# Performance work log

Hardware: AMD Instinct MI355X
Metric: run time of the kernel (lower is better)

## Reference

```python
import jax, jax.numpy as jnp
import numpy as np

N_NODES = 50000
N_EDGES = 800000
IN_DIM = 256
NHID = 64
OUT_DIM = 64
DEPTH = 4
P = 2.0


def _gcn_conv(x, W, b, src, dst, n):
    # PyG GCNConv: xW, add self-loops, sym-normalize, aggregate src->dst, + bias
    xw = x @ W
    loop = jnp.arange(n)
    s = jnp.concatenate([src, loop])
    d = jnp.concatenate([dst, loop])
    deg = jax.ops.segment_sum(jnp.ones_like(d, dtype=xw.dtype), d, num_segments=n)
    dis = jnp.where(deg > 0, jax.lax.rsqrt(jnp.maximum(deg, 1.0)), 0.0)
    w = dis[s] * dis[d]  # [E+n]
    out = jax.ops.segment_sum(w[:, None] * xw[s], d, num_segments=n)
    return out + b


def _g2_gate(x, W, b, src, dst, n):
    xg = jax.nn.relu(_gcn_conv(x, W, b, src, dst, n))
    diff = jnp.abs(xg[src] - xg[dst]) ** P  # [E, nhid]
    sums = jax.ops.segment_sum(diff, src, num_segments=n)
    cnt = jax.ops.segment_sum(jnp.ones((src.shape[0],), dtype=x.dtype), src, num_segments=n)
    return jnp.tanh(sums / jnp.maximum(cnt, 1.0)[:, None])


def setup_inputs() -> dict:
    key = jax.random.key(0)
    ks = jax.random.split(key, 10)
    x = jax.random.normal(ks[0], (N_NODES, IN_DIM), dtype=jnp.float32)
    edge_index = jax.random.randint(ks[1], (2, N_EDGES), 0, N_NODES, dtype=jnp.int64 if jax.config.jax_enable_x64 else jnp.int32)
    s = 0.05
    return {
        "x": x,
        "edge_index": edge_index,
        "enc_w": jax.random.normal(ks[2], (IN_DIM, NHID), dtype=jnp.float32) * s,
        "enc_b": jnp.zeros((NHID,), dtype=jnp.float32),
        "conv_w": jax.random.normal(ks[3], (NHID, NHID), dtype=jnp.float32) * s,
        "conv_b": jnp.zeros((NHID,), dtype=jnp.float32),
        "gg_w": jax.random.normal(ks[4], (NHID, NHID), dtype=jnp.float32) * s,
        "gg_b": jnp.zeros((NHID,), dtype=jnp.float32),
        "dec_w": jax.random.normal(ks[5], (NHID, OUT_DIM), dtype=jnp.float32) * s,
        "dec_b": jnp.zeros((OUT_DIM,), dtype=jnp.float32),
    }


def reference(x, edge_index, enc_w, enc_b, conv_w, conv_b, gg_w, gg_b, dec_w, dec_b):
    n = x.shape[0]
    src, dst = edge_index[0], edge_index[1]
    # eval mode: dropouts are identity
    X = jax.nn.relu(x @ enc_w + enc_b)
    for _ in range(DEPTH):
        X_ = jax.nn.relu(_gcn_conv(X, conv_w, conv_b, src, dst, n))
        tau = _g2_gate(X, gg_w, gg_b, src, dst, n)
        X = (1.0 - tau) * X + tau * X_
    X = jax.nn.relu(X @ dec_w + dec_b)
    return X
```

## Files before the change

### kernel.cpp

```cpp
#include <hip/hip_runtime.h>
#include <math.h>

#define NN 50000
#define NE 800000
#define IND 256
#define NH 64
#define DEPTH 4
#define PART_DIV 6250
#define SB 49
#define EPP 100000


__device__ __forceinline__ unsigned short f2bf(float f) {
    unsigned int x = __float_as_uint(f);
    unsigned int r = (x + 0x7fffu + ((x >> 16) & 1u)) >> 16;
    return (unsigned short)r;
}
__device__ __forceinline__ unsigned int pack2bf(float lo, float hi) {
    return (unsigned int)f2bf(lo) | ((unsigned int)f2bf(hi) << 16);
}
__device__ __forceinline__ ushort4 f4_to_us4(float4 f) {
    ushort4 u;
    u.x = f2bf(f.x); u.y = f2bf(f.y); u.z = f2bf(f.z); u.w = f2bf(f.w);
    return u;
}
__device__ __forceinline__ void acc8(float* a, uint4 r) {
    a[0] += __uint_as_float(r.x << 16); a[1] += __uint_as_float(r.x & 0xffff0000u);
    a[2] += __uint_as_float(r.y << 16); a[3] += __uint_as_float(r.y & 0xffff0000u);
    a[4] += __uint_as_float(r.z << 16); a[5] += __uint_as_float(r.z & 0xffff0000u);
    a[6] += __uint_as_float(r.w << 16); a[7] += __uint_as_float(r.w & 0xffff0000u);
}
__device__ __forceinline__ void unpack8(float* a, uint4 r) {
    a[0] = __uint_as_float(r.x << 16); a[1] = __uint_as_float(r.x & 0xffff0000u);
    a[2] = __uint_as_float(r.y << 16); a[3] = __uint_as_float(r.y & 0xffff0000u);
    a[4] = __uint_as_float(r.z << 16); a[5] = __uint_as_float(r.z & 0xffff0000u);
    a[6] = __uint_as_float(r.w << 16); a[7] = __uint_as_float(r.w & 0xffff0000u);
}
__device__ __forceinline__ void accd8(float* a, const float* xg, uint4 r) {
    float e;
    e = xg[0] - __uint_as_float(r.x << 16);         a[0] += e * e;
    e = xg[1] - __uint_as_float(r.x & 0xffff0000u); a[1] += e * e;
    e = xg[2] - __uint_as_float(r.y << 16);         a[2] += e * e;
    e = xg[3] - __uint_as_float(r.y & 0xffff0000u); a[3] += e * e;
    e = xg[4] - __uint_as_float(r.z << 16);         a[4] += e * e;
    e = xg[5] - __uint_as_float(r.z & 0xffff0000u); a[5] += e * e;
    e = xg[6] - __uint_as_float(r.w << 16);         a[6] += e * e;
    e = xg[7] - __uint_as_float(r.w & 0xffff0000u); a[7] += e * e;
}
__device__ __forceinline__ float tanh_pos(float x) {
    float t = __expf(-2.f * x);
    return (1.f - t) / (1.f + t);
}


__global__ void count8(const int* __restrict__ src, const int* __restrict__ dst,
                       int* __restrict__ hin, int* __restrict__ hout,
                       int* __restrict__ lrin, int* __restrict__ lrout,
                       int nGroups) {
    int p = blockIdx.x & 7;
    int g = blockIdx.x >> 3;
    int* hi = hin + p * NN;
    int* ho = hout + p * NN;
    for (int i = g * 256 + threadIdx.x; i < EPP; i += nGroups * 256) {
        int e = p * EPP + i;
        int s = src[e], d = dst[e];
        lrin[e]  = atomicAdd(&hi[d], 1);
        lrout[e] = atomicAdd(&ho[s], 1);
    }
}

__global__ void reduce8(int* __restrict__ hin, int* __restrict__ hout,
                        int* __restrict__ degin, int* __restrict__ degout) {
    int i = blockIdx.x * blockDim.x + threadIdx.x;
    if (i >= NN) return;
    int run = 0;
#pragma unroll
    for (int p = 0; p < 8; ++p) {
        int t = hin[p * NN + i]; hin[p * NN + i] = run; run += t;
    }
    degin[i] = run;
    run = 0;
#pragma unroll
    for (int p = 0; p < 8; ++p) {
        int t = hout[p * NN + i]; hout[p * NN + i] = run; run += t;
    }
    degout[i] = run;
}

__global__ __launch_bounds__(512) void scan_p1(const int* __restrict__ in0,
                                               const int* __restrict__ in1,
                                               int* __restrict__ tmp,
                                               int* __restrict__ bsum) {
    int a = blockIdx.x / SB;
    int b = blockIdx.x % SB;
    const int* in = a ? in1 : in0;
    int t = threadIdx.x;
    int base = b * 1024 + t * 2;
    int v0 = (base < NN) ? in[base] : 0;
    int v1 = (base + 1 < NN) ? in[base + 1] : 0;
    int v = v0 + v1;
    int x = v;
#pragma unroll
    for (int off = 1; off < 64; off <<= 1) {
        int u = __shfl_up(x, off);
        if ((t & 63) >= off) x += u;
    }
    __shared__ int ws[8];
    int wid = t >> 6, lane = t & 63;
    if (lane == 63) ws[wid] = x;
    __syncthreads();
    if (t == 0) {
        int run = 0;
#pragma unroll
        for (int w = 0; w < 8; ++w) { int s = ws[w]; ws[w] = run; run += s; }
    }
    __syncthreads();
    x += ws[wid];
    int excl = x - v;
    if (base < NN) tmp[a * NN + base] = excl;
    if (base + 1 < NN) tmp[a * NN + base + 1] = excl + v0;
    if (t == 511) bsum[a * SB + b] = x;
}

__global__ __launch_bounds__(128) void scan_p2(int* __restrict__ bsum,
                                               int* __restrict__ out0,
                                               int* __restrict__ out1) {
    int t = threadIdx.x;
    int a = t >> 6, lane = t & 63;
    int v = (lane < SB) ? bsum[a * SB + lane] : 0;
    int x = v;
#pragma unroll
    for (int off = 1; off < 64; off <<= 1) {
        int u = __shfl_up(x, off);
        if (lane >= off) x += u;
    }
    if (lane < SB) bsum[a * SB + lane] = x - v;
    if (lane == SB - 1) {
        if (a == 0) out0[NN] = x; else out1[NN] = x;
    }
}

__global__ __launch_bounds__(512) void scan_p3(const int* __restrict__ tmp,
                                               const int* __restrict__ bsum,
                                               int* __restrict__ out0,
                                               int* __restrict__ out1) {
    int a = blockIdx.x / SB;
    int b = blockIdx.x % SB;
    int* out = a ? out1 : out0;
    int add = bsum[a * SB + b];
    int t = threadIdx.x;
    int base = b * 1024 + t * 2;
    if (base < NN) out[base] = tmp[a * NN + base] + add;
    if (base + 1 < NN) out[base + 1] = tmp[a * NN + base + 1] + add;
}

__global__ void init_node(const int* __restrict__ degin, const int* __restrict__ degout,
                          float* __restrict__ dis, float* __restrict__ cntf) {
    int i = blockIdx.x * blockDim.x + threadIdx.x;
    if (i < NN) {
        dis[i] = rsqrtf((float)(degin[i] + 1));
        int od = degout[i];
        cntf[i] = (float)(od > 0 ? od : 1);
    }
}

__global__ void fill_csr_part(const int* __restrict__ src, const int* __restrict__ dst,
                              const int* __restrict__ off_dst, const int* __restrict__ off_src,
                              const int* __restrict__ hin, const int* __restrict__ hout,
                              const int* __restrict__ lrin, const int* __restrict__ lrout,
                              int* __restrict__ srcs_by_dst, int* __restrict__ dsts_by_src,
                              int nGroups) {
    int q = blockIdx.x & 7;
    int g = blockIdx.x >> 3;
    for (int pe = 0; pe < 8; ++pe) {
        const int* bin = hin + pe * NN;
        const int* bout = hout + pe * NN;
        for (int i = g * 256 + threadIdx.x; i < EPP; i += nGroups * 256) {
            int e = pe * EPP + i;
            int s = src[e], d = dst[e];
            if (d / PART_DIV == q) srcs_by_dst[off_dst[d] + bin[d] + lrin[e]] = s;
            if (s / PART_DIV == q) dsts_by_src[off_src[s] + bout[s] + lrout[e]] = d;
        }
    }
}

template<int K, bool RELU, bool WSC>
__global__ __launch_bounds__(256) void gemm64b(const float* __restrict__ X,
                                               const float* __restrict__ W,
                                               const float* __restrict__ bias,
                                               const float* __restrict__ rowscale,
                                               float* __restrict__ out,
                                               unsigned short* __restrict__ xsc, int n) {
    __shared__ float Ws[64 * 64];
    __shared__ float Xs[64][68];
    int tid = threadIdx.x;
    int row0 = blockIdx.x * 64;
    int r16 = tid >> 4;
    int cg = tid & 15;
    float4 acc[4];
#pragma unroll
    for (int t = 0; t < 4; ++t) acc[t] = make_float4(0.f, 0.f, 0.f, 0.f);

    for (int kc = 0; kc < K; kc += 64) {
        const float4* W4 = (const float4*)(W + (size_t)kc * 64);
        float4* Ws4 = (float4*)Ws;
#pragma unroll
        for (int t = 0; t < 4; ++t) Ws4[tid + t * 256] = W4[tid + t * 256];
#pragma unroll
        for (int t = 0; t < 4; ++t) {
            int r = r16 + t * 16;
            int grow = row0 + r;
            float4 xv = make_float4(0.f, 0.f, 0.f, 0.f);
            if (grow < n) xv = *(const float4*)(X + (size_t)grow * K + kc + cg * 4);
            Xs[r][cg * 4 + 0] = xv.x; Xs[r][cg * 4 + 1] = xv.y;
            Xs[r][cg * 4 + 2] = xv.z; Xs[r][cg * 4 + 3] = xv.w;
        }
        __syncthreads();
#pragma unroll
        for (int k = 0; k < 64; ++k) {
            float4 w4 = ((const float4*)Ws)[k * 16 + cg];
#pragma unroll
            for (int t = 0; t < 4; ++t) {
                float xv = Xs[r16 + t * 16][k];
                acc[t].x += xv * w4.x; acc[t].y += xv * w4.y;
                acc[t].z += xv * w4.z; acc[t].w += xv * w4.w;
            }
        }
        __syncthreads();
    }

    float4 b4 = ((const float4*)bias)[cg];
#pragma unroll
    for (int t = 0; t < 4; ++t) {
        int row = row0 + r16 + t * 16;
        if (row < n) {
            float4 o;
            o.x = acc[t].x + b4.x; o.y = acc[t].y + b4.y;
            o.z = acc[t].z + b4.z; o.w = acc[t].w + b4.w;
            if (RELU) {
                o.x = fmaxf(o.x, 0.f); o.y = fmaxf(o.y, 0.f);
                o.z = fmaxf(o.z, 0.f); o.w = fmaxf(o.w, 0.f);
            }
            ((float4*)(out + (size_t)row * 64))[cg] = o;
            if (WSC) {
                float s = rowscale[row];
                float4 o2 = make_float4(o.x * s, o.y * s, o.z * s, o.w * s);
                ((ushort4*)(xsc + (size_t)row * 64))[cg] = f4_to_us4(o2);
            }
        }
    }
}

template<bool OUTBF>
__global__ __launch_bounds__(256) void gemm64z(const float* __restrict__ Z,
                                               const float* __restrict__ W,
                                               const float* __restrict__ bias,
                                               float* __restrict__ outf,
                                               unsigned short* __restrict__ outb, int n) {
    __shared__ float Ws[64 * 64];
    __shared__ float Xs[64][68];
    int tid = threadIdx.x;
    int row0 = blockIdx.x * 64;
    int r16 = tid >> 4;
    int cg = tid & 15;
    float4 acc[4];
#pragma unroll
    for (int t = 0; t < 4; ++t) acc[t] = make_float4(0.f, 0.f, 0.f, 0.f);

    {
        const float4* W4 = (const float4*)W;
        float4* Ws4 = (float4*)Ws;
#pragma unroll
        for (int t = 0; t < 4; ++t) Ws4[tid + t * 256] = W4[tid + t * 256];
#pragma unroll
        for (int t = 0; t < 4; ++t) {
            int r = r16 + t * 16;
            int gr = row0 + r;
            float4 xv = make_float4(0.f, 0.f, 0.f, 0.f);
            if (gr < n) xv = *(const float4*)(Z + (size_t)gr * 64 + cg * 4);
            Xs[r][cg * 4 + 0] = xv.x; Xs[r][cg * 4 + 1] = xv.y;
            Xs[r][cg * 4 + 2] = xv.z; Xs[r][cg * 4 + 3] = xv.w;
        }
        __syncthreads();
#pragma unroll
        for (int k = 0; k < 64; ++k) {
            float4 w4 = ((const float4*)Ws)[k * 16 + cg];
#pragma unroll
            for (int t = 0; t < 4; ++t) {
                float xv = Xs[r16 + t * 16][k];
                acc[t].x += xv * w4.x; acc[t].y += xv * w4.y;
                acc[t].z += xv * w4.z; acc[t].w += xv * w4.w;
            }
        }
    }

    float4 b4 = ((const float4*)bias)[cg];
#pragma unroll
    for (int t = 0; t < 4; ++t) {
        int row = row0 + r16 + t * 16;
        if (row < n) {
            float4 o;
            o.x = fmaxf(acc[t].x + b4.x, 0.f); o.y = fmaxf(acc[t].y + b4.y, 0.f);
            o.z = fmaxf(acc[t].z + b4.z, 0.f); o.w = fmaxf(acc[t].w + b4.w, 0.f);
            if (OUTBF) {
                ((ushort4*)(outb + (size_t)row * 64))[cg] = f4_to_us4(o);
            } else {
                ((float4*)(outf + (size_t)row * 64))[cg] = o;
            }
        }
    }
}

__global__ __launch_bounds__(256) void zgather(
    const unsigned short* __restrict__ Xbf,
    const int* __restrict__ off, const int* __restrict__ nbr,
    const float* __restrict__ dis, float* __restrict__ Z)
{
    int t = blockIdx.x * 256 + threadIdx.x;
    int node = t >> 3, l8 = t & 7;
    if (node >= NN) return;
    int lane = threadIdx.x & 63;
    int octbase = lane & ~7;
    const uint4* Xb = (const uint4*)Xbf;
    float a[8];
    unpack8(a, Xb[(size_t)node * 8 + l8]);
    int lo = off[node], hi = off[node + 1];
    int j = lo;
    for (; j + 7 < hi; j += 8) {
        int nv = nbr[j + l8];
        int s0 = __shfl(nv, octbase + 0), s1 = __shfl(nv, octbase + 1);
        int s2 = __shfl(nv, octbase + 2), s3 = __shfl(nv, octbase + 3);
        int s4 = __shfl(nv, octbase + 4), s5 = __shfl(nv, octbase + 5);
        int s6 = __shfl(nv, octbase + 6), s7 = __shfl(nv, octbase + 7);
        uint4 r0 = Xb[(size_t)s0 * 8 + l8];
        uint4 r1 = Xb[(size_t)s1 * 8 + l8];
        uint4 r2 = Xb[(size_t)s2 * 8 + l8];
        uint4 r3 = Xb[(size_t)s3 * 8 + l8];
        uint4 r4 = Xb[(size_t)s4 * 8 + l8];
        uint4 r5 = Xb[(size_t)s5 * 8 + l8];
        uint4 r6 = Xb[(size_t)s6 * 8 + l8];
        uint4 r7 = Xb[(size_t)s7 * 8 + l8];
        acc8(a, r0); acc8(a, r1); acc8(a, r2); acc8(a, r3);
        acc8(a, r4); acc8(a, r5); acc8(a, r6); acc8(a, r7);
    }
    for (; j + 3 < hi; j += 4) {
        int s0 = nbr[j], s1 = nbr[j + 1], s2 = nbr[j + 2], s3 = nbr[j + 3];
        uint4 r0 = Xb[(size_t)s0 * 8 + l8];
        uint4 r1 = Xb[(size_t)s1 * 8 + l8];
        uint4 r2 = Xb[(size_t)s2 * 8 + l8];
        uint4 r3 = Xb[(size_t)s3 * 8 + l8];
        acc8(a, r0); acc8(a, r1); acc8(a, r2); acc8(a, r3);
    }
    for (; j < hi; ++j) {
        acc8(a, Xb[(size_t)nbr[j] * 8 + l8]);
    }
    float di = dis[node];
    float* zp = Z + (size_t)node * 64 + l8 * 8;
    *(float4*)(zp)     = make_float4(di * a[0], di * a[1], di * a[2], di * a[3]);
    *(float4*)(zp + 4) = make_float4(di * a[4], di * a[5], di * a[6], di * a[7]);
}

__global__ __launch_bounds__(256) void gate_update8(
    const unsigned short* __restrict__ Cbf, const float* __restrict__ Xn,
    float* __restrict__ X, unsigned short* __restrict__ Xbf,
    const int* __restrict__ off, const int* __restrict__ nbr,
    const float* __restrict__ cntf, const float* __restrict__ dis)
{
    int t = blockIdx.x * 256 + threadIdx.x;
    int node = t >> 3, l8 = t & 7;
    if (node >= NN) return;
    int lane = threadIdx.x & 63;
    int octbase = lane & ~7;
    const uint4* Cb = (const uint4*)Cbf;
    float xg[8];
    unpack8(xg, Cb[(size_t)node * 8 + l8]);
    float a[8] = {0.f, 0.f, 0.f, 0.f, 0.f, 0.f, 0.f, 0.f};
    int lo = off[node], hi = off[node + 1];
    int j = lo;
    for (; j + 7 < hi; j += 8) {
        int nv = nbr[j + l8];
        int d0 = __shfl(nv, octbase + 0), d1 = __shfl(nv, octbase + 1);
        int d2 = __shfl(nv, octbase + 2), d3 = __shfl(nv, octbase + 3);
        int d4 = __shfl(nv, octbase + 4), d5 = __shfl(nv, octbase + 5);
        int d6 = __shfl(nv, octbase + 6), d7 = __shfl(nv, octbase + 7);
        uint4 r0 = Cb[(size_t)d0 * 8 + l8];
        uint4 r1 = Cb[(size_t)d1 * 8 + l8];
        uint4 r2 = Cb[(size_t)d2 * 8 + l8];
        uint4 r3 = Cb[(size_t)d3 * 8 + l8];
        uint4 r4 = Cb[(size_t)d4 * 8 + l8];
        uint4 r5 = Cb[(size_t)d5 * 8 + l8];
        uint4 r6 = Cb[(size_t)d6 * 8 + l8];
        uint4 r7 = Cb[(size_t)d7 * 8 + l8];
        accd8(a, xg, r0); accd8(a, xg, r1); accd8(a, xg, r2); accd8(a, xg, r3);
        accd8(a, xg, r4); accd8(a, xg, r5); accd8(a, xg, r6); accd8(a, xg, r7);
    }
    for (; j + 3 < hi; j += 4) {
        int d0 = nbr[j], d1 = nbr[j + 1], d2 = nbr[j + 2], d3 = nbr[j + 3];
        uint4 r0 = Cb[(size_t)d0 * 8 + l8];
        uint4 r1 = Cb[(size_t)d1 * 8 + l8];
        uint4 r2 = Cb[(size_t)d2 * 8 + l8];
        uint4 r3 = Cb[(size_t)d3 * 8 + l8];
        accd8(a, xg, r0); accd8(a, xg, r1); accd8(a, xg, r2); accd8(a, xg, r3);
    }
    for (; j < hi; ++j) {
        accd8(a, xg, Cb[(size_t)nbr[j] * 8 + l8]);
    }
    float inv = 1.f / cntf[node];
    float di = dis[node];
    const float* xop = X + (size_t)node * 64 + l8 * 8;
    const float* xnp = Xn + (size_t)node * 64 + l8 * 8;
    float o[8];
#pragma unroll
    for (int k = 0; k < 8; ++k) {
        float tau = tanh_pos(a[k] * inv);
        float xo = xop[k], xn = xnp[k];
        o[k] = xo + tau * (xn - xo);
    }
    float* xp = X + (size_t)node * 64 + l8 * 8;
    *(float4*)(xp)     = make_float4(o[0], o[1], o[2], o[3]);
    *(float4*)(xp + 4) = make_float4(o[4], o[5], o[6], o[7]);
    uint4 pk;
    pk.x = pack2bf(o[0] * di, o[1] * di);
    pk.y = pack2bf(o[2] * di, o[3] * di);
    pk.z = pack2bf(o[4] * di, o[5] * di);
    pk.w = pack2bf(o[6] * di, o[7] * di);
    ((uint4*)Xbf)[(size_t)node * 8 + l8] = pk;
}


extern "C" void kernel_launch(void* const* d_in, const int* in_sizes, int n_in,
                              void* d_out, int out_size, void* d_ws, size_t ws_size,
                              hipStream_t stream) {
    const float* x      = (const float*)d_in[0];
    const int*   ei     = (const int*)d_in[1];
    const float* enc_w  = (const float*)d_in[2];
    const float* enc_b  = (const float*)d_in[3];
    const float* conv_w = (const float*)d_in[4];
    const float* conv_b = (const float*)d_in[5];
    const float* gg_w   = (const float*)d_in[6];
    const float* gg_b   = (const float*)d_in[7];
    const float* dec_w  = (const float*)d_in[8];
    const float* dec_b  = (const float*)d_in[9];
    float* out = (float*)d_out;

    const int* src = ei;
    const int* dst = ei + NE;

    char* p = (char*)d_ws;
    auto alloc = [&](size_t bytes) -> void* {
        void* r = (void*)p;
        p += (bytes + 255) & ~(size_t)255;
        return r;
    };
    float* X   = (float*)alloc((size_t)NN * 64 * 4);
    float* Zb  = (float*)alloc((size_t)NN * 64 * 4);
    float* B   = (float*)alloc((size_t)NN * 64 * 4);
    unsigned short* Xbf = (unsigned short*)alloc((size_t)NN * 64 * 2);
    unsigned short* Cbf = (unsigned short*)alloc((size_t)NN * 64 * 2);
    float* dis  = (float*)alloc((size_t)NN * 4);
    float* cntf = (float*)alloc((size_t)NN * 4);
    int* degin   = (int*)alloc((size_t)NN * 4);
    int* degout  = (int*)alloc((size_t)NN * 4);
    int* off_dst = (int*)alloc((size_t)(NN + 1) * 4);
    int* off_src = (int*)alloc((size_t)(NN + 1) * 4);
    int* hin     = (int*)alloc((size_t)8 * NN * 4);
    int* hout    = (int*)alloc((size_t)8 * NN * 4);
    int* lrin    = (int*)alloc((size_t)NE * 4);
    int* lrout   = (int*)alloc((size_t)NE * 4);
    int* sbd     = (int*)alloc((size_t)NE * 4);
    int* dbs     = (int*)alloc((size_t)NE * 4);
    int* stmp    = (int*)alloc((size_t)2 * NN * 4);
    int* bsum    = (int*)alloc((size_t)2 * SB * 4);

    hipMemsetAsync(hin, 0, (size_t)8 * NN * 4, stream);
    hipMemsetAsync(hout, 0, (size_t)8 * NN * 4, stream);

    const int NB = (NN + 255) / 256;
    const int NGROUPS = 104;
    count8<<<8 * NGROUPS, 256, 0, stream>>>(src, dst, hin, hout, lrin, lrout, NGROUPS);
    reduce8<<<NB, 256, 0, stream>>>(hin, hout, degin, degout);
    scan_p1<<<2 * SB, 512, 0, stream>>>(degin, degout, stmp, bsum);
    scan_p2<<<1, 128, 0, stream>>>(bsum, off_dst, off_src);
    scan_p3<<<2 * SB, 512, 0, stream>>>(stmp, bsum, off_dst, off_src);
    init_node<<<NB, 256, 0, stream>>>(degin, degout, dis, cntf);
    fill_csr_part<<<8 * NGROUPS, 256, 0, stream>>>(src, dst, off_dst, off_src,
                                                   hin, hout, lrin, lrout,
                                                   sbd, dbs, NGROUPS);

    const int GB = (NN + 63) / 64;
    const int OB = ((NN * 8) + 255) / 256;

    gemm64b<IND, true, true><<<GB, 256, 0, stream>>>(x, enc_w, enc_b, dis, X, Xbf, NN);

    for (int l = 0; l < DEPTH; ++l) {
        zgather<<<OB, 256, 0, stream>>>(Xbf, off_dst, sbd, dis, Zb);
        gemm64z<false><<<GB, 256, 0, stream>>>(Zb, conv_w, conv_b, B, nullptr, NN);
        gemm64z<true><<<GB, 256, 0, stream>>>(Zb, gg_w, gg_b, nullptr, Cbf, NN);
        gate_update8<<<OB, 256, 0, stream>>>(Cbf, B, X, Xbf, off_src, dbs, cntf, dis);
    }

    gemm64b<NH, true, false><<<GB, 256, 0, stream>>>(X, dec_w, dec_b, nullptr, out, nullptr, NN);
}
```

Before: 685.2 us.

## Degree-sort node order for gathers, fuse dual GEMM, store B in bf16

Measured after the change: 651.8 us. 1.05x faster.

```diff
diff --git a/kernel.cpp b/kernel.cpp
--- a/kernel.cpp
+++ b/kernel.cpp
@@ -184,6 +184,61 @@
     }
 }
 
+__global__ void bucket_hist(const int* __restrict__ degin, const int* __restrict__ degout,
+                            int* __restrict__ ghin, int* __restrict__ ghout) {
+    __shared__ int lin[128], lout[128];
+    int t = threadIdx.x;
+    if (t < 128) { lin[t] = 0; lout[t] = 0; }
+    __syncthreads();
+    int i = blockIdx.x * 256 + t;
+    if (i < NN) {
+        atomicAdd(&lin[min(degin[i], 127)], 1);
+        atomicAdd(&lout[min(degout[i], 127)], 1);
+    }
+    __syncthreads();
+    if (t < 128) {
+        if (lin[t])  atomicAdd(&ghin[t],  lin[t]);
+        if (lout[t]) atomicAdd(&ghout[t], lout[t]);
+    }
+}
+
+__global__ void bucket_scan(const int* __restrict__ ghin, const int* __restrict__ ghout,
+                            int* __restrict__ curin, int* __restrict__ curout) {
+    __shared__ int a[128], b[128];
+    int t = threadIdx.x;
+    if (t < 128) a[t] = ghin[t]; else b[t - 128] = ghout[t - 128];
+    __syncthreads();
+    if (t == 0) { int run = 0; for (int k = 0; k < 128; ++k) { int v = a[k]; a[k] = run; run += v; } }
+    if (t == 1) { int run = 0; for (int k = 0; k < 128; ++k) { int v = b[k]; b[k] = run; run += v; } }
+    __syncthreads();
+    if (t < 128) curin[t] = a[t]; else curout[t - 128] = b[t - 128];
+}
+
+__global__ void bucket_scatter(const int* __restrict__ degin, const int* __restrict__ degout,
+                               int* __restrict__ curin, int* __restrict__ curout,
+                               int* __restrict__ order_in, int* __restrict__ order_out) {
+    __shared__ int lin[128], lout[128], basein[128], baseout[128];
+    int t = threadIdx.x;
+    if (t < 128) { lin[t] = 0; lout[t] = 0; }
+    __syncthreads();
+    int i = blockIdx.x * 256 + t;
+    int bi = 0, bo = 0, ri = 0, ro = 0;
+    if (i < NN) {
+        bi = min(degin[i], 127);  ri = atomicAdd(&lin[bi], 1);
+        bo = min(degout[i], 127); ro = atomicAdd(&lout[bo], 1);
+    }
+    __syncthreads();
+    if (t < 128) {
+        basein[t]  = lin[t]  ? atomicAdd(&curin[t],  lin[t])  : 0;
+        baseout[t] = lout[t] ? atomicAdd(&curout[t], lout[t]) : 0;
+    }
+    __syncthreads();
+    if (i < NN) {
+        order_in[basein[bi] + ri] = i;
+        order_out[baseout[bo] + ro] = i;
+    }
+}
+
 template<int K, bool RELU, bool WSC>
 __global__ __launch_bounds__(256) void gemm64b(const float* __restrict__ X,
                                                const float* __restrict__ W,
@@ -251,62 +306,65 @@
     }
 }
 
-template<bool OUTBF>
-__global__ __launch_bounds__(256) void gemm64z(const float* __restrict__ Z,
-                                               const float* __restrict__ W,
-                                               const float* __restrict__ bias,
-                                               float* __restrict__ outf,
-                                               unsigned short* __restrict__ outb, int n) {
-    __shared__ float Ws[64 * 64];
-    __shared__ float Xs[64][68];
+__global__ __launch_bounds__(256) void dualgemm32(
+    const float* __restrict__ Z,
+    const float* __restrict__ Wb, const float* __restrict__ bb,
+    const float* __restrict__ Wc, const float* __restrict__ bc,
+    unsigned short* __restrict__ Bbf, unsigned short* __restrict__ Cbf, int n)
+{
+    __shared__ float W2[64 * 128];
+    __shared__ float Xs[32][68];
     int tid = threadIdx.x;
-    int row0 = blockIdx.x * 64;
-    int r16 = tid >> 4;
-    int cg = tid & 15;
-    float4 acc[4];
-#pragma unroll
-    for (int t = 0; t < 4; ++t) acc[t] = make_float4(0.f, 0.f, 0.f, 0.f);
-
+    int row0 = blockIdx.x * 32;
     {
-        const float4* W4 = (const float4*)W;
-        float4* Ws4 = (float4*)Ws;
-#pragma unroll
-        for (int t = 0; t < 4; ++t) Ws4[tid + t * 256] = W4[tid + t * 256];
+        const float4* wb4 = (const float4*)Wb;
+        const float4* wc4 = (const float4*)Wc;
 #pragma unroll
         for (int t = 0; t < 4; ++t) {
-            int r = r16 + t * 16;
+            int idx = tid + t * 256;
+            int k = idx >> 4, c = (idx & 15) * 4;
+            *(float4*)&W2[k * 128 + c]      = wb4[idx];
+            *(float4*)&W2[k * 128 + 64 + c] = wc4[idx];
+        }
+#pragma unroll
+        for (int t = 0; t < 2; ++t) {
+            int idx = tid + t * 256;
+            int r = idx >> 4, c4 = idx & 15;
             int gr = row0 + r;
             float4 xv = make_float4(0.f, 0.f, 0.f, 0.f);
-            if (gr < n) xv = *(const float4*)(Z + (size_t)gr * 64 + cg * 4);
-            Xs[r][cg * 4 + 0] = xv.x; Xs[r][cg * 4 + 1] = xv.y;
-            Xs[r][cg * 4 + 2] = xv.z; Xs[r][cg * 4 + 3] = xv.w;
-        }
-        __syncthreads();
-#pragma unroll
-        for (int k = 0; k < 64; ++k) {
-            float4 w4 = ((const float4*)Ws)[k * 16 + cg];
-#pragma unroll
-            for (int t = 0; t < 4; ++t) {
-                float xv = Xs[r16 + t * 16][k];
-                acc[t].x += xv * w4.x; acc[t].y += xv * w4.y;
-                acc[t].z += xv * w4.z; acc[t].w += xv * w4.w;
-            }
-        }
-    }
-
-    float4 b4 = ((const float4*)bias)[cg];
+            if (gr < n) xv = *(const float4*)(Z + (size_t)gr * 64 + c4 * 4);
+            Xs[r][c4 * 4 + 0] = xv.x; Xs[r][c4 * 4 + 1] = xv.y;
+            Xs[r][c4 * 4 + 2] = xv.z; Xs[r][c4 * 4 + 3] = xv.w;
+        }
+    }
+    __syncthreads();
+
+    int r8 = tid >> 5;
+    int cg = tid & 31;
+    float4 acc[4];
+#pragma unroll
+    for (int t = 0; t < 4; ++t) acc[t] = make_float4(0.f, 0.f, 0.f, 0.f);
+#pragma unroll
+    for (int k = 0; k < 64; ++k) {
+        float4 w4 = *(const float4*)&W2[k * 128 + cg * 4];
+#pragma unroll
+        for (int t = 0; t < 4; ++t) {
+            float xv = Xs[r8 + t * 8][k];
+            acc[t].x += xv * w4.x; acc[t].y += xv * w4.y;
+            acc[t].z += xv * w4.z; acc[t].w += xv * w4.w;
+        }
+    }
+
+    float4 bv = (cg < 16) ? ((const float4*)bb)[cg] : ((const float4*)bc)[cg - 16];
 #pragma unroll
     for (int t = 0; t < 4; ++t) {
-        int row = row0 + r16 + t * 16;
+        int row = row0 + r8 + t * 8;
         if (row < n) {
             float4 o;
-            o.x = fmaxf(acc[t].x + b4.x, 0.f); o.y = fmaxf(acc[t].y + b4.y, 0.f);
-            o.z = fmaxf(acc[t].z + b4.z, 0.f); o.w = fmaxf(acc[t].w + b4.w, 0.f);
-            if (OUTBF) {
-                ((ushort4*)(outb + (size_t)row * 64))[cg] = f4_to_us4(o);
-            } else {
-                ((float4*)(outf + (size_t)row * 64))[cg] = o;
-            }
+            o.x = fmaxf(acc[t].x + bv.x, 0.f); o.y = fmaxf(acc[t].y + bv.y, 0.f);
+            o.z = fmaxf(acc[t].z + bv.z, 0.f); o.w = fmaxf(acc[t].w + bv.w, 0.f);
+            if (cg < 16) ((ushort4*)(Bbf + (size_t)row * 64))[cg]      = f4_to_us4(o);
+            else         ((ushort4*)(Cbf + (size_t)row * 64))[cg - 16] = f4_to_us4(o);
         }
     }
 }
@@ -314,24 +372,21 @@
 __global__ __launch_bounds__(256) void zgather(
     const unsigned short* __restrict__ Xbf,
     const int* __restrict__ off, const int* __restrict__ nbr,
-    const float* __restrict__ dis, float* __restrict__ Z)
+    const float* __restrict__ dis, const int* __restrict__ order,
+    float* __restrict__ Z)
 {
     int t = blockIdx.x * 256 + threadIdx.x;
-    int node = t >> 3, l8 = t & 7;
-    if (node >= NN) return;
-    int lane = threadIdx.x & 63;
-    int octbase = lane & ~7;
+    int idx = t >> 3, l8 = t & 7;
+    if (idx >= NN) return;
+    int node = order[idx];
     const uint4* Xb = (const uint4*)Xbf;
     float a[8];
     unpack8(a, Xb[(size_t)node * 8 + l8]);
     int lo = off[node], hi = off[node + 1];
     int j = lo;
     for (; j + 7 < hi; j += 8) {
-        int nv = nbr[j + l8];
-        int s0 = __shfl(nv, octbase + 0), s1 = __shfl(nv, octbase + 1);
-        int s2 = __shfl(nv, octbase + 2), s3 = __shfl(nv, octbase + 3);
-        int s4 = __shfl(nv, octbase + 4), s5 = __shfl(nv, octbase + 5);
-        int s6 = __shfl(nv, octbase + 6), s7 = __shfl(nv, octbase + 7);
+        int s0 = nbr[j],     s1 = nbr[j + 1], s2 = nbr[j + 2], s3 = nbr[j + 3];
+        int s4 = nbr[j + 4], s5 = nbr[j + 5], s6 = nbr[j + 6], s7 = nbr[j + 7];
         uint4 r0 = Xb[(size_t)s0 * 8 + l8];
         uint4 r1 = Xb[(size_t)s1 * 8 + l8];
         uint4 r2 = Xb[(size_t)s2 * 8 + l8];
@@ -361,16 +416,16 @@
 }
 
 __global__ __launch_bounds__(256) void gate_update8(
-    const unsigned short* __restrict__ Cbf, const float* __restrict__ Xn,
+    const unsigned short* __restrict__ Cbf, const unsigned short* __restrict__ Xnbf,
     float* __restrict__ X, unsigned short* __restrict__ Xbf,
     const int* __restrict__ off, const int* __restrict__ nbr,
-    const float* __restrict__ cntf, const float* __restrict__ dis)
+    const float* __restrict__ cntf, const float* __restrict__ dis,
+    const int* __restrict__ order)
 {
     int t = blockIdx.x * 256 + threadIdx.x;
-    int node = t >> 3, l8 = t & 7;
-    if (node >= NN) return;
-    int lane = threadIdx.x & 63;
-    int octbase = lane & ~7;
+    int idx = t >> 3, l8 = t & 7;
+    if (idx >= NN) return;
+    int node = order[idx];
     const uint4* Cb = (const uint4*)Cbf;
     float xg[8];
     unpack8(xg, Cb[(size_t)node * 8 + l8]);
@@ -378,11 +433,8 @@
     int lo = off[node], hi = off[node + 1];
     int j = lo;
     for (; j + 7 < hi; j += 8) {
-        int nv = nbr[j + l8];
-        int d0 = __shfl(nv, octbase + 0), d1 = __shfl(nv, octbase + 1);
-        int d2 = __shfl(nv, octbase + 2), d3 = __shfl(nv, octbase + 3);
-        int d4 = __shfl(nv, octbase + 4), d5 = __shfl(nv, octbase + 5);
-        int d6 = __shfl(nv, octbase + 6), d7 = __shfl(nv, octbase + 7);
+        int d0 = nbr[j],     d1 = nbr[j + 1], d2 = nbr[j + 2], d3 = nbr[j + 3];
+        int d4 = nbr[j + 4], d5 = nbr[j + 5], d6 = nbr[j + 6], d7 = nbr[j + 7];
         uint4 r0 = Cb[(size_t)d0 * 8 + l8];
         uint4 r1 = Cb[(size_t)d1 * 8 + l8];
         uint4 r2 = Cb[(size_t)d2 * 8 + l8];
@@ -407,14 +459,15 @@
     }
     float inv = 1.f / cntf[node];
     float di = dis[node];
+    float xn[8];
+    unpack8(xn, ((const uint4*)Xnbf)[(size_t)node * 8 + l8]);
     const float* xop = X + (size_t)node * 64 + l8 * 8;
-    const float* xnp = Xn + (size_t)node * 64 + l8 * 8;
     float o[8];
 #pragma unroll
     for (int k = 0; k < 8; ++k) {
         float tau = tanh_pos(a[k] * inv);
-        float xo = xop[k], xn = xnp[k];
-        o[k] = xo + tau * (xn - xo);
+        float xo = xop[k];
+        o[k] = xo + tau * (xn[k] - xo);
     }
     float* xp = X + (size_t)node * 64 + l8 * 8;
     *(float4*)(xp)     = make_float4(o[0], o[1], o[2], o[3]);
@@ -454,7 +507,7 @@
     };
     float* X   = (float*)alloc((size_t)NN * 64 * 4);
     float* Zb  = (float*)alloc((size_t)NN * 64 * 4);
-    float* B   = (float*)alloc((size_t)NN * 64 * 4);
+    unsigned short* Bbf = (unsigned short*)alloc((size_t)NN * 64 * 2);
     unsigned short* Xbf = (unsigned short*)alloc((size_t)NN * 64 * 2);
     unsigned short* Cbf = (unsigned short*)alloc((size_t)NN * 64 * 2);
     float* dis  = (float*)alloc((size_t)NN * 4);
@@ -471,9 +524,14 @@
     int* dbs     = (int*)alloc((size_t)NE * 4);
     int* stmp    = (int*)alloc((size_t)2 * NN * 4);
     int* bsum    = (int*)alloc((size_t)2 * SB * 4);
+    int* order_in  = (int*)alloc((size_t)NN * 4);
+    int* order_out = (int*)alloc((size_t)NN * 4);
+    int* gbins   = (int*)alloc((size_t)512 * 4);
+    int* ghin = gbins, *ghout = gbins + 128, *curin = gbins + 256, *curout = gbins + 384;
 
     hipMemsetAsync(hin, 0, (size_t)8 * NN * 4, stream);
     hipMemsetAsync(hout, 0, (size_t)8 * NN * 4, stream);
+    hipMemsetAsync(gbins, 0, (size_t)512 * 4, stream);
 
     const int NB = (NN + 255) / 256;
     const int NGROUPS = 104;
@@ -483,20 +541,25 @@
     scan_p2<<<1, 128, 0, stream>>>(bsum, off_dst, off_src);
     scan_p3<<<2 * SB, 512, 0, stream>>>(stmp, bsum, off_dst, off_src);
     init_node<<<NB, 256, 0, stream>>>(degin, degout, dis, cntf);
+    bucket_hist<<<NB, 256, 0, stream>>>(degin, degout, ghin, ghout);
+    bucket_scan<<<1, 256, 0, stream>>>(ghin, ghout, curin, curout);
+    bucket_scatter<<<NB, 256, 0, stream>>>(degin, degout, curin, curout,
+                                           order_in, order_out);
     fill_csr_part<<<8 * NGROUPS, 256, 0, stream>>>(src, dst, off_dst, off_src,
                                                    hin, hout, lrin, lrout,
                                                    sbd, dbs, NGROUPS);
 
-    const int GB = (NN + 63) / 64;
-    const int OB = ((NN * 8) + 255) / 256;
+    const int GB   = (NN + 63) / 64;
+    const int GB32 = (NN + 31) / 32;
+    const int OB   = ((NN * 8) + 255) / 256;
 
     gemm64b<IND, true, true><<<GB, 256, 0, stream>>>(x, enc_w, enc_b, dis, X, Xbf, NN);
 
     for (int l = 0; l < DEPTH; ++l) {
-        zgather<<<OB, 256, 0, stream>>>(Xbf, off_dst, sbd, dis, Zb);
-        gemm64z<false><<<GB, 256, 0, stream>>>(Zb, conv_w, conv_b, B, nullptr, NN);
-        gemm64z<true><<<GB, 256, 0, stream>>>(Zb, gg_w, gg_b, nullptr, Cbf, NN);
-        gate_update8<<<OB, 256, 0, stream>>>(Cbf, B, X, Xbf, off_src, dbs, cntf, dis);
+        zgather<<<OB, 256, 0, stream>>>(Xbf, off_dst, sbd, dis, order_in, Zb);
+        dualgemm32<<<GB32, 256, 0, stream>>>(Zb, conv_w, conv_b, gg_w, gg_b, Bbf, Cbf, NN);
+        gate_update8<<<OB, 256, 0, stream>>>(Cbf, Bbf, X, Xbf, off_src, dbs,
+                                             cntf, dis, order_out);
     }
 
     gemm64b<NH, true, false><<<GB, 256, 0, stream>>>(X, dec_w, dec_b, nullptr, out, nullptr, NN);
```
